# Kernel optimization log

Hardware: AMD Instinct MI355X
Metric: run time of the kernel (lower is better)

The kernel has to match this reference:

```python
import jax, jax.numpy as jnp
import numpy as np

B, N, C = 8, 4096, 640
H_HEADS = 5
HD = C // H_HEADS  # 128
KS = 5
FOCUS = 3.0
EPS = 1e-6


def setup_inputs() -> dict:
    key = jax.random.key(0)
    ks = jax.random.split(key, 12)
    s = 0.02
    return {
        "x1": jax.random.normal(ks[0], (B, N, C), jnp.float32),
        "x2": jax.random.normal(ks[1], (B, N, C), jnp.float32),
        "Wq": jax.random.normal(ks[2], (C, C), jnp.float32) * s,
        "Wkv": jax.random.normal(ks[3], (2 * C, C), jnp.float32) * s,
        "Wproj": jax.random.normal(ks[4], (C, C), jnp.float32) * s,
        "bproj": jax.random.normal(ks[5], (C,), jnp.float32) * s,
        "dwc_w": jax.random.normal(ks[6], (HD, 1, KS, KS), jnp.float32) * s,
        "dwc_b": jax.random.normal(ks[7], (HD,), jnp.float32) * s,
        "scale": jax.random.normal(ks[8], (1, 1, C), jnp.float32) * s,
        "pos_enc": jax.random.normal(ks[9], (1, N, C), jnp.float32) * s,
        "H": 64,
        "W": 64,
    }


def _split_heads(t):
    # [B, N, C] -> [(B*h), N, hd]
    b, n, c = t.shape
    return t.reshape(b, n, H_HEADS, HD).transpose(0, 2, 1, 3).reshape(b * H_HEADS, n, HD)


def reference(x1, x2, Wq, Wkv, Wproj, bproj, dwc_w, dwc_b, scale, pos_enc, H, W):
    b, n, c = x1.shape
    # note the module's naming swap: self.q projects x2 into v
    v = x2 @ Wq.T                               # [B,N,C]
    kv = (x1 @ Wkv.T).reshape(b, n, 2, c)       # sr_ratio == 1 path
    k = kv[:, :, 0, :] + pos_enc
    q = kv[:, :, 1, :]

    sc = jax.nn.softplus(scale)                 # [1,1,C]
    q = (jax.nn.relu(q) + EPS) / sc
    k = (jax.nn.relu(k) + EPS) / sc
    q_norm = jnp.linalg.norm(q, axis=-1, keepdims=True)
    k_norm = jnp.linalg.norm(k, axis=-1, keepdims=True)
    q = q ** FOCUS
    k = k ** FOCUS
    q = q / jnp.linalg.norm(q, axis=-1, keepdims=True) * q_norm
    k = k / jnp.linalg.norm(k, axis=-1, keepdims=True) * k_norm

    q, k, v = _split_heads(q), _split_heads(k), _split_heads(v)  # [(B*h), N, hd]
    i, j, cc, d = q.shape[-2], k.shape[-2], k.shape[-1], v.shape[-1]
    z = 1.0 / (jnp.einsum('bic,bc->bi', q, k.sum(axis=1)) + EPS)  # [(B*h), N]
    if i * j * (cc + d) > cc * d * (i + j):
        kv2 = jnp.einsum('bjc,bjd->bcd', k, v)                    # [(B*h), hd, hd]
        x = jnp.einsum('bic,bcd,bi->bid', q, kv2, z)
    else:
        qk = jnp.einsum('bic,bjc->bij', q, k)
        x = jnp.einsum('bij,bjd,bi->bid', qk, v, z)

    # depthwise conv feature map on v: 'b (w h) c -> b c w h'
    num = int(round(n ** 0.5))
    fm = v.reshape(v.shape[0], num, num, HD).transpose(0, 3, 1, 2)  # [(B*h), hd, num, num]
    fm = jax.lax.conv_general_dilated(
        fm, dwc_w, window_strides=(1, 1), padding=((KS // 2, KS // 2),) * 2,
        dimension_numbers=('NCHW', 'OIHW', 'NCHW'), feature_group_count=HD)
    fm = fm + dwc_b[None, :, None, None]
    fm = fm.transpose(0, 2, 3, 1).reshape(v.shape[0], n, HD)

    x = x + fm
    # '(b h) n c -> b n (h c)'
    x = x.reshape(b, H_HEADS, n, HD).transpose(0, 2, 1, 3).reshape(b, n, c)
    return x @ Wproj.T + bproj
```

## Files before the change

kernel.cpp:

```cpp
#include <hip/hip_runtime.h>
#include <math.h>

constexpr int CB  = 8;
constexpr int CN  = 4096;
constexpr int CC  = 640;
constexpr int CNH = 5;
constexpr int CHD = 128;
constexpr int CM  = CB * CN;
constexpr float CEPS = 1e-6f;
constexpr int NCH = 8;

typedef __attribute__((ext_vector_type(8))) short bf16x8;
typedef __attribute__((ext_vector_type(4))) float f32x4;

typedef __attribute__((address_space(1))) const unsigned int gas_u32;
typedef __attribute__((address_space(3))) unsigned int las_u32;

__device__ __forceinline__ void gload16(const void* g, void* l) {
    __builtin_amdgcn_global_load_lds((gas_u32*)g, (las_u32*)l, 16, 0, 0);
}

__device__ __forceinline__ short f2bf(float x) {
    unsigned u = __float_as_uint(x);
    unsigned r = (u + 0x7fffu + ((u >> 16) & 1u)) >> 16;
    return (short)r;
}
__device__ __forceinline__ float b2f(unsigned short u) {
    return __uint_as_float(((unsigned)u) << 16);
}

__device__ __forceinline__ void cvt8(const float* __restrict__ s, unsigned short* __restrict__ d) {
    float4 f0 = *(const float4*)s, f1 = *(const float4*)(s + 4);
    bf16x8 h;
    h[0]=f2bf(f0.x); h[1]=f2bf(f0.y); h[2]=f2bf(f0.z); h[3]=f2bf(f0.w);
    h[4]=f2bf(f1.x); h[5]=f2bf(f1.y); h[6]=f2bf(f1.z); h[7]=f2bf(f1.w);
    *(bf16x8*)d = h;
}

__global__ __launch_bounds__(256) void prep_weights(const float* __restrict__ scale,
                                                    const float* __restrict__ Wq,
                                                    const float* __restrict__ Wkv,
                                                    const float* __restrict__ Wproj,
                                                    float* __restrict__ sc,
                                                    unsigned short* __restrict__ Wqbf,
                                                    unsigned short* __restrict__ Wkvbf,
                                                    unsigned short* __restrict__ Wprojbf) {
    const int gid = blockIdx.x * 256 + threadIdx.x;
    if (gid < CC) sc[gid] = log1pf(expf(scale[gid]));
    const int NQ = CC * CC / 8;
    const int NKV = 2 * CC * CC / 8;
    const int total = NQ + NKV + NQ;
    const int stride = gridDim.x * 256;
    for (int c = gid; c < total; c += stride) {
        if (c < NQ)            cvt8(Wq    + (size_t)c * 8,            Wqbf    + (size_t)c * 8);
        else if (c < NQ + NKV) cvt8(Wkv   + (size_t)(c - NQ) * 8,     Wkvbf   + (size_t)(c - NQ) * 8);
        else                   cvt8(Wproj + (size_t)(c - NQ - NKV) * 8, Wprojbf + (size_t)(c - NQ - NKV) * 8);
    }
}

__global__ __launch_bounds__(256) void cvt_x12(const float* __restrict__ x1,
                                               const float* __restrict__ x2,
                                               unsigned short* __restrict__ x1bf,
                                               unsigned short* __restrict__ x2bf,
                                               int n8) {
    int i = blockIdx.x * 256 + threadIdx.x;
    const int stride = gridDim.x * 256;
    for (; i < 2 * n8; i += stride) {
        if (i < n8) cvt8(x1 + (size_t)i * 8,        x1bf + (size_t)i * 8);
        else        cvt8(x2 + (size_t)(i - n8) * 8, x2bf + (size_t)(i - n8) * 8);
    }
}

template<bool BIAS, bool OUTBF>
__device__ __forceinline__ void gemm_core(const unsigned short* __restrict__ Abf,
                                          const unsigned short* __restrict__ Bbf,
                                          void* __restrict__ Co,
                                          const float* __restrict__ bias,
                                          int Kr, int Nr, int wg, int npan, int mper) {
    __shared__ unsigned short lA[2][4096];
    __shared__ unsigned short lB[2][4096];
    const int t  = threadIdx.x;
    const int xcd  = wg & 7;
    const int j    = wg >> 3;
    const int m0 = (xcd * mper + j / npan) * 128;
    const int n0 = (j % npan) * 128;
    const int l  = t & 63, w = t >> 6, wr = w >> 1, wc = w & 1;

    const int cp0 = w * 64 + l;
    const int cp1 = cp0 + 256;
    const int s0 = cp0 ^ (((cp0 >> 2) & 7) ^ ((cp0 >> 4) & 1));
    const int s1 = cp1 ^ (((cp1 >> 2) & 7) ^ ((cp1 >> 4) & 1));
    const size_t gA0 = (size_t)(m0 + (s0 >> 2)) * Kr + (s0 & 3) * 8;
    const size_t gA1 = (size_t)(m0 + (s1 >> 2)) * Kr + (s1 & 3) * 8;
    const size_t gB0 = (size_t)(n0 + (s0 >> 2)) * Kr + (s0 & 3) * 8;
    const size_t gB1 = (size_t)(n0 + (s1 >> 2)) * Kr + (s1 & 3) * 8;
    const int dA0 = w * 512;
    const int dA1 = 2048 + w * 512;

    const int offA = ((wr * 64 + (l & 15)) * 64 + (l >> 4) * 16) ^ ((l & 7) << 4);
    const int offB = ((wc * 64 + (l & 15)) * 64 + (l >> 4) * 16) ^ ((l & 7) << 4);

    f32x4 acc[4][4];
    #pragma unroll
    for (int i = 0; i < 4; ++i)
        #pragma unroll
        for (int j2 = 0; j2 < 4; ++j2) acc[i][j2] = (f32x4){0.f, 0.f, 0.f, 0.f};

    gload16(Abf + gA0, &lA[0][dA0]);
    gload16(Abf + gA1, &lA[0][dA1]);
    gload16(Bbf + gB0, &lB[0][dA0]);
    gload16(Bbf + gB1, &lB[0][dA1]);
    __syncthreads();

    int cur = 0;
    for (int k0 = 0; k0 < Kr; k0 += 32) {
        if (k0 + 32 < Kr) {
            const int nb = cur ^ 1;
            gload16(Abf + gA0 + k0 + 32, &lA[nb][dA0]);
            gload16(Abf + gA1 + k0 + 32, &lA[nb][dA1]);
            gload16(Bbf + gB0 + k0 + 32, &lB[nb][dA0]);
            gload16(Bbf + gB1 + k0 + 32, &lB[nb][dA1]);
        }
        bf16x8 af[4], bfv[4];
        #pragma unroll
        for (int i = 0; i < 4; ++i) {
            af[i]  = *(const bf16x8*)((const char*)&lA[cur][0] + offA + i * 1024);
            bfv[i] = *(const bf16x8*)((const char*)&lB[cur][0] + offB + i * 1024);
        }
        #pragma unroll
        for (int i = 0; i < 4; ++i)
            #pragma unroll
            for (int j2 = 0; j2 < 4; ++j2)
                acc[i][j2] = __builtin_amdgcn_mfma_f32_16x16x32_bf16(af[i], bfv[j2], acc[i][j2], 0, 0, 0);
        __syncthreads();
        cur ^= 1;
    }

    #pragma unroll
    for (int j2 = 0; j2 < 4; ++j2) {
        const int n = n0 + wc * 64 + j2 * 16 + (l & 15);
        const float bv = BIAS ? bias[n] : 0.f;
        #pragma unroll
        for (int i = 0; i < 4; ++i) {
            const int m = m0 + wr * 64 + i * 16 + (l >> 4) * 4;
            #pragma unroll
            for (int r = 0; r < 4; ++r) {
                float val = acc[i][j2][r] + bv;
                if (OUTBF) ((unsigned short*)Co)[(size_t)(m + r) * Nr + n] = (unsigned short)f2bf(val);
                else       ((float*)Co)[(size_t)(m + r) * Nr + n] = val;
            }
        }
    }
}

__global__ __launch_bounds__(256) void gemm_vkq(const unsigned short* __restrict__ x2bf,
                                                const unsigned short* __restrict__ Wqbf,
                                                unsigned short* __restrict__ vbf,
                                                const unsigned short* __restrict__ x1bf,
                                                const unsigned short* __restrict__ Wkvbf,
                                                unsigned short* __restrict__ kqbf) {
    const int id = blockIdx.x;
    if (id < 1280) {
        gemm_core<false, true>(x2bf, Wqbf, (void*)vbf, nullptr, CC, CC, id, 5, 32);
    } else {
        gemm_core<false, true>(x1bf, Wkvbf, (void*)kqbf, nullptr, CC, 1280, id - 1280, 10, 32);
    }
}

__global__ __launch_bounds__(256) void gemm_proj(const unsigned short* __restrict__ xbf,
                                                 const unsigned short* __restrict__ Wprojbf,
                                                 float* __restrict__ out,
                                                 const float* __restrict__ bproj) {
    gemm_core<true, false>(xbf, Wprojbf, (void*)out, bproj, CC, CC,
                           blockIdx.y * gridDim.x + blockIdx.x, gridDim.x, gridDim.y >> 3);
}

__global__ __launch_bounds__(256) void rowtrans2(const unsigned short* __restrict__ kq,
                                                 const float* __restrict__ pos,
                                                 const float* __restrict__ sc,
                                                 unsigned short* __restrict__ qt,
                                                 unsigned short* __restrict__ kt) {
    const int w = threadIdx.x >> 6, l = threadIdx.x & 63;
    const int m = blockIdx.x * 4 + w;
    const int n = m & (CN - 1);
    const unsigned short* rowk = kq + (size_t)m * 1280;
    const unsigned short* rowq = rowk + 640;
    float qv[10], kv[10];
    float s2q = 0.f, s6q = 0.f, s2k = 0.f, s6k = 0.f;
    #pragma unroll
    for (int j = 0; j < 10; ++j) {
        const int c = l + 64 * j;
        const float scv = sc[c];
        float qq = (fmaxf(b2f(rowq[c]), 0.f) + CEPS) / scv;
        float kk = (fmaxf(b2f(rowk[c]) + pos[(size_t)n * CC + c], 0.f) + CEPS) / scv;
        qv[j] = qq; kv[j] = kk;
        const float q2 = qq * qq, k2 = kk * kk;
        s2q += q2; s6q += q2 * q2 * q2;
        s2k += k2; s6k += k2 * k2 * k2;
    }
    #pragma unroll
    for (int o = 32; o > 0; o >>= 1) {
        s2q += __shfl_xor(s2q, o);
        s6q += __shfl_xor(s6q, o);
        s2k += __shfl_xor(s2k, o);
        s6k += __shfl_xor(s6k, o);
    }
    const float qmul = sqrtf(s2q) / sqrtf(s6q);
    const float kmul = sqrtf(s2k) / sqrtf(s6k);
    #pragma unroll
    for (int j = 0; j < 10; ++j) {
        const int c = l + 64 * j;
        qt[(size_t)m * CC + c] = (unsigned short)f2bf(qv[j] * qv[j] * qv[j] * qmul);
        kt[(size_t)m * CC + c] = (unsigned short)f2bf(kv[j] * kv[j] * kv[j] * kmul);
    }
}

__global__ __launch_bounds__(256) void kv2_partial(const unsigned short* __restrict__ kt,
                                                   const unsigned short* __restrict__ vb,
                                                   float* __restrict__ kv2p,
                                                   float* __restrict__ ksmp) {
    const int nc = blockIdx.x, bh = blockIdx.y, q = blockIdx.z;
    const int qc = q & 1, qd = q >> 1;
    const int b = bh / CNH, h = bh % CNH;
    __shared__ float ks[32][68];
    __shared__ float vs[32][68];
    const int t = threadIdx.x;
    const int tx = t & 15, ty = t >> 4;
    float acc[4][4];
    #pragma unroll
    for (int i = 0; i < 4; ++i)
        #pragma unroll
        for (int j = 0; j < 4; ++j) acc[i][j] = 0.f;
    float ksacc = 0.f;
    const size_t mbase = (size_t)b * CN + (size_t)nc * 512;
    const int cofK = h * CHD + qc * 64;
    const int cofV = h * CHD + qd * 64;
    const int token = t >> 3, c8 = (t & 7) * 8;
    for (int tile = 0; tile < 16; ++tile) {
        const int nt0 = tile * 32;
        __syncthreads();
        {
            const size_t r = (mbase + nt0 + token) * CC;
            bf16x8 hk = *(const bf16x8*)(kt + r + cofK + c8);
            bf16x8 hv = *(const bf16x8*)(vb + r + cofV + c8);
            float4 k0, k1, v0, v1;
            k0.x=b2f(hk[0]); k0.y=b2f(hk[1]); k0.z=b2f(hk[2]); k0.w=b2f(hk[3]);
            k1.x=b2f(hk[4]); k1.y=b2f(hk[5]); k1.z=b2f(hk[6]); k1.w=b2f(hk[7]);
            v0.x=b2f(hv[0]); v0.y=b2f(hv[1]); v0.z=b2f(hv[2]); v0.w=b2f(hv[3]);
            v1.x=b2f(hv[4]); v1.y=b2f(hv[5]); v1.z=b2f(hv[6]); v1.w=b2f(hv[7]);
            *(float4*)&ks[token][c8]     = k0;
            *(float4*)&ks[token][c8 + 4] = k1;
            *(float4*)&vs[token][c8]     = v0;
            *(float4*)&vs[token][c8 + 4] = v1;
        }
        __syncthreads();
        #pragma unroll 4
        for (int nn = 0; nn < 32; ++nn) {
            float4 av = *(const float4*)&ks[nn][ty * 4];
            float4 bv = *(const float4*)&vs[nn][tx * 4];
            float a[4] = {av.x, av.y, av.z, av.w};
            float bb[4] = {bv.x, bv.y, bv.z, bv.w};
            #pragma unroll
            for (int i = 0; i < 4; ++i)
                #pragma unroll
                for (int j = 0; j < 4; ++j)
                    acc[i][j] = fmaf(a[i], bb[j], acc[i][j]);
        }
        if (qd == 0 && t < 64) {
            #pragma unroll
            for (int nn = 0; nn < 32; ++nn) ksacc += ks[nn][t];
        }
    }
    float* outp = kv2p + (((size_t)bh * NCH + nc) * 4 + q) * 4096;
    #pragma unroll
    for (int i = 0; i < 4; ++i) {
        float4 o;
        o.x = acc[i][0]; o.y = acc[i][1]; o.z = acc[i][2]; o.w = acc[i][3];
        *(float4*)&outp[(ty * 4 + i) * 64 + tx * 4] = o;
    }
    if (qd == 0 && t < 64)
        ksmp[(((size_t)bh * NCH + nc) * 2 + qc) * 64 + t] = ksacc;
}

__global__ __launch_bounds__(256) void kv2_reduce(const float* __restrict__ kv2p,
                                                  const float* __restrict__ ksmp,
                                                  unsigned short* __restrict__ kv2bf,
                                                  float* __restrict__ ksm) {
    const int bh = blockIdx.x, t = threadIdx.x;
    for (int o = t; o < 16384; o += 256) {
        const int d = o >> 7, c = o & 127;
        const int q = (d >> 6) * 2 + (c >> 6);
        float s = 0.f;
        #pragma unroll
        for (int nc = 0; nc < NCH; ++nc)
            s += kv2p[(((size_t)bh * NCH + nc) * 4 + q) * 4096 + (c & 63) * 64 + (d & 63)];
        kv2bf[(size_t)bh * 16384 + o] = (unsigned short)f2bf(s);
    }
    if (t < 128) {
        float s = 0.f;
        #pragma unroll
        for (int nc = 0; nc < NCH; ++nc)
            s += ksmp[(((size_t)bh * NCH + nc) * 2 + (t >> 6)) * 64 + (t & 63)];
        ksm[(size_t)bh * 128 + t] = s;
    }
}

__global__ __launch_bounds__(256) void attn_mfma(const unsigned short* __restrict__ qt,
                                                 const unsigned short* __restrict__ kv2bf,
                                                 const float* __restrict__ ksm,
                                                 unsigned short* __restrict__ attb) {
    const int nb = blockIdx.x, bh = blockIdx.y;
    const int b = bh / CNH, h = bh % CNH;
    __shared__ short lQ[16384];
    __shared__ short lKV[16384];
    __shared__ float zs[128];
    const int t = threadIdx.x;
    const int l = t & 63, w = t >> 6, wr = w >> 1, wc = w & 1;
    const size_t m0 = (size_t)b * CN + (size_t)nb * 128;

    const int srow0 = t >> 4;
    const int c16   = t & 15;
    float kreg[8];
    {
        const float* kp = ksm + (size_t)bh * 128 + c16 * 8;
        float4 k0 = *(const float4*)kp, k1 = *(const float4*)(kp + 4);
        kreg[0]=k0.x; kreg[1]=k0.y; kreg[2]=k0.z; kreg[3]=k0.w;
        kreg[4]=k1.x; kreg[5]=k1.y; kreg[6]=k1.z; kreg[7]=k1.w;
    }
    #pragma unroll
    for (int p = 0; p < 8; ++p) {
        const int row = srow0 + p * 16;
        const int st = (row * 256 + c16 * 16) ^ ((row & 7) << 4);
        bf16x8 hq = *(const bf16x8*)(qt + (m0 + row) * CC + h * CHD + c16 * 8);
        *(bf16x8*)((char*)lQ + st) = hq;
        float zp = 0.f;
        #pragma unroll
        for (int j = 0; j < 8; ++j) zp = fmaf(b2f((unsigned short)hq[j]), kreg[j], zp);
        zp += __shfl_xor(zp, 1);
        zp += __shfl_xor(zp, 2);
        zp += __shfl_xor(zp, 4);
        zp += __shfl_xor(zp, 8);
        if (c16 == 0) zs[row] = 1.f / (zp + CEPS);
        bf16x8 hk = *(const bf16x8*)(kv2bf + (size_t)bh * 16384 + row * 128 + c16 * 8);
        *(bf16x8*)((char*)lKV + st) = hk;
    }
    __syncthreads();

    const int baseA = (wr * 64 + (l & 15)) * 256 + ((l >> 4) << 4);
    const int baseB = (wc * 64 + (l & 15)) * 256 + ((l >> 4) << 4);
    const int xorv  = (l & 7) << 4;
    f32x4 acc[4][4];
    #pragma unroll
    for (int i = 0; i < 4; ++i)
        #pragma unroll
        for (int j = 0; j < 4; ++j) acc[i][j] = (f32x4){0.f, 0.f, 0.f, 0.f};

    #pragma unroll
    for (int kk = 0; kk < 4; ++kk) {
        bf16x8 af[4], bv[4];
        #pragma unroll
        for (int i = 0; i < 4; ++i) {
            af[i] = *(const bf16x8*)((const char*)lQ  + (((baseA + kk * 64) ^ xorv) + i * 4096));
            bv[i] = *(const bf16x8*)((const char*)lKV + (((baseB + kk * 64) ^ xorv) + i * 4096));
        }
        #pragma unroll
        for (int i = 0; i < 4; ++i)
            #pragma unroll
            for (int j = 0; j < 4; ++j)
                acc[i][j] = __builtin_amdgcn_mfma_f32_16x16x32_bf16(af[i], bv[j], acc[i][j], 0, 0, 0);
    }

    #pragma unroll
    for (int i = 0; i < 4; ++i) {
        const int mBase = wr * 64 + i * 16 + (l >> 4) * 4;
        float zv[4];
        #pragma unroll
        for (int r = 0; r < 4; ++r) zv[r] = zs[mBase + r];
        #pragma unroll
        for (int j = 0; j < 4; ++j) {
            const int n = wc * 64 + j * 16 + (l & 15);
            unsigned short* op = attb + (m0 + mBase) * CC + h * CHD + n;
            #pragma unroll
            for (int r = 0; r < 4; ++r)
                op[(size_t)r * CC] = (unsigned short)f2bf(acc[i][j][r] * zv[r]);
        }
    }
}

__global__ __launch_bounds__(256) void dwconv2(const unsigned short* __restrict__ vb,
                                               const unsigned short* __restrict__ attb,
                                               const float* __restrict__ w,
                                               const float* __restrict__ bias,
                                               unsigned short* __restrict__ xb) {
    const int yt = blockIdx.x;
    const int dq = blockIdx.y;
    const int bh = blockIdx.z;
    const int b = bh / CNH, h = bh % CNH;
    __shared__ unsigned short vt[12 * 68 * 32];
    const int t = threadIdx.x;
    const int y0 = yt * 8;
    const size_t rowbase = (size_t)b * CN;
    const int cbase = h * CHD + dq * 32;
    for (int c = t; c < 3264; c += 256) {
        int pos = c >> 2, d8 = (c & 3) * 8;
        int ly = pos / 68, lx = pos - ly * 68;
        int yy = y0 - 2 + ly, xx = lx - 2;
        bf16x8 val = (bf16x8){0,0,0,0,0,0,0,0};
        if (yy >= 0 && yy < 64 && xx >= 0 && xx < 64)
            val = *(const bf16x8*)(vb + (rowbase + yy * 64 + xx) * CC + cbase + d8);
        *(bf16x8*)(vt + pos * 32 + d8) = val;
    }
    __syncthreads();
    const int dp = t & 15;
    const int xg = t >> 4;
    const int d0 = dq * 32 + dp * 2;
    float wr0[25], wr1[25];
    #pragma unroll
    for (int i = 0; i < 25; ++i) {
        wr0[i] = w[d0 * 25 + i];
        wr1[i] = w[(d0 + 1) * 25 + i];
    }
    const float bv0 = bias[d0], bv1 = bias[d0 + 1];
    const int x0 = xg * 4;
    for (int oy = 0; oy < 8; ++oy) {
        float a0[4] = {bv0, bv0, bv0, bv0}, a1[4] = {bv1, bv1, bv1, bv1};
        #pragma unroll
        for (int dy = 0; dy < 5; ++dy) {
            const unsigned short* rp = vt + ((oy + dy) * 68 + x0) * 32 + dp * 2;
            float v0[8], v1[8];
            #pragma unroll
            for (int j = 0; j < 8; ++j) {
                unsigned pr = *(const unsigned*)(rp + j * 32);
                v0[j] = __uint_as_float(pr << 16);
                v1[j] = __uint_as_float(pr & 0xffff0000u);
            }
            #pragma unroll
            for (int dx = 0; dx < 5; ++dx) {
                const float w0 = wr0[dy * 5 + dx], w1 = wr1[dy * 5 + dx];
                #pragma unroll
                for (int xo = 0; xo < 4; ++xo) {
                    a0[xo] = fmaf(w0, v0[xo + dx], a0[xo]);
                    a1[xo] = fmaf(w1, v1[xo + dx], a1[xo]);
                }
            }
        }
        #pragma unroll
        for (int xo = 0; xo < 4; ++xo) {
            size_t g = (rowbase + (y0 + oy) * 64 + x0 + xo) * CC + cbase + dp * 2;
            unsigned ap = *(const unsigned*)(attb + g);
            float at0 = __uint_as_float(ap << 16);
            float at1 = __uint_as_float(ap & 0xffff0000u);
            unsigned short o0 = (unsigned short)f2bf(a0[xo] + at0);
            unsigned short o1 = (unsigned short)f2bf(a1[xo] + at1);
            *(unsigned*)(xb + g) = (unsigned)o0 | ((unsigned)o1 << 16);
        }
    }
}

extern "C" void kernel_launch(void* const* d_in, const int* in_sizes, int n_in,
                              void* d_out, int out_size, void* d_ws, size_t ws_size,
                              hipStream_t stream) {
    (void)in_sizes; (void)n_in; (void)out_size; (void)ws_size;
    const float* x1    = (const float*)d_in[0];
    const float* x2    = (const float*)d_in[1];
    const float* Wq    = (const float*)d_in[2];
    const float* Wkv   = (const float*)d_in[3];
    const float* Wproj = (const float*)d_in[4];
    const float* bproj = (const float*)d_in[5];
    const float* dwcw  = (const float*)d_in[6];
    const float* dwcb  = (const float*)d_in[7];
    const float* scale = (const float*)d_in[8];
    const float* pos   = (const float*)d_in[9];
    float* out = (float*)d_out;

    const size_t MC = (size_t)CM * CC;
    unsigned short* ws16 = (unsigned short*)d_ws;
    unsigned short* x1bf  = ws16;
    float*          kv2p  = (float*)ws16;
    unsigned short* attbf = ws16;
    unsigned short* x2bf = ws16 + MC;
    unsigned short* ktbf = x2bf;
    unsigned short* xbf  = x2bf;
    unsigned short* vbf  = ws16 + 2 * MC;
    unsigned short* qtbf = ws16 + 3 * MC;
    unsigned short* kv2bf = ws16 + 4 * MC;
    float* ksmp = (float*)(kv2bf + (size_t)40 * 16384);
    float* ksm  = ksmp + (size_t)40 * NCH * 128;
    float* scb  = ksm + (size_t)40 * 128;
    unsigned short* Wqbf    = (unsigned short*)(scb + 640);
    unsigned short* Wkvbf   = Wqbf + (size_t)CC * CC;
    unsigned short* Wprojbf = Wkvbf + (size_t)2 * CC * CC;
    unsigned short* kqbf = (unsigned short*)d_out;

    hipLaunchKernelGGL(prep_weights, dim3(256), dim3(256), 0, stream,
                       scale, Wq, Wkv, Wproj, scb, Wqbf, Wkvbf, Wprojbf);
    hipLaunchKernelGGL(cvt_x12, dim3(2048), dim3(256), 0, stream,
                       x1, x2, x1bf, x2bf, (int)(MC / 8));

    hipLaunchKernelGGL(gemm_vkq, dim3(3840), dim3(256), 0, stream,
                       x2bf, Wqbf, vbf, x1bf, Wkvbf, kqbf);
    hipLaunchKernelGGL(rowtrans2, dim3(CM/4), dim3(256), 0, stream, kqbf, pos, scb, qtbf, ktbf);
    hipLaunchKernelGGL(kv2_partial, dim3(NCH, 40, 4), dim3(256), 0, stream, ktbf, vbf, kv2p, ksmp);
    hipLaunchKernelGGL(kv2_reduce, dim3(40), dim3(256), 0, stream, kv2p, ksmp, kv2bf, ksm);
    hipLaunchKernelGGL(attn_mfma, dim3(CN/128, 40), dim3(256), 0, stream, qtbf, kv2bf, ksm, attbf);
    hipLaunchKernelGGL(dwconv2, dim3(8, 4, 40), dim3(256), 0, stream, vbf, attbf, dwcw, dwcb, xbf);
    hipLaunchKernelGGL(gemm_proj, dim3(CC/128, CM/128), dim3(256), 0, stream,
                       xbf, Wprojbf, out, bproj);
}
```

Measured before the change: 479.7 us.

## Fuse q/k feature-map transform into consumers, store only per-row norm factors

```diff
diff --git a/kernel.cpp b/kernel.cpp
--- a/kernel.cpp
+++ b/kernel.cpp
@@ -175,17 +175,16 @@
                            blockIdx.y * gridDim.x + blockIdx.x, gridDim.x, gridDim.y >> 3);
 }
 
-__global__ __launch_bounds__(256) void rowtrans2(const unsigned short* __restrict__ kq,
-                                                 const float* __restrict__ pos,
-                                                 const float* __restrict__ sc,
-                                                 unsigned short* __restrict__ qt,
-                                                 unsigned short* __restrict__ kt) {
+__global__ __launch_bounds__(256) void rowfact(const unsigned short* __restrict__ kq,
+                                               const float* __restrict__ pos,
+                                               const float* __restrict__ sc,
+                                               float* __restrict__ qf,
+                                               float* __restrict__ kf) {
     const int w = threadIdx.x >> 6, l = threadIdx.x & 63;
     const int m = blockIdx.x * 4 + w;
     const int n = m & (CN - 1);
     const unsigned short* rowk = kq + (size_t)m * 1280;
     const unsigned short* rowq = rowk + 640;
-    float qv[10], kv[10];
     float s2q = 0.f, s6q = 0.f, s2k = 0.f, s6k = 0.f;
     #pragma unroll
     for (int j = 0; j < 10; ++j) {
@@ -193,7 +192,6 @@
         const float scv = sc[c];
         float qq = (fmaxf(b2f(rowq[c]), 0.f) + CEPS) / scv;
         float kk = (fmaxf(b2f(rowk[c]) + pos[(size_t)n * CC + c], 0.f) + CEPS) / scv;
-        qv[j] = qq; kv[j] = kk;
         const float q2 = qq * qq, k2 = kk * kk;
         s2q += q2; s6q += q2 * q2 * q2;
         s2k += k2; s6k += k2 * k2 * k2;
@@ -205,18 +203,17 @@
         s2k += __shfl_xor(s2k, o);
         s6k += __shfl_xor(s6k, o);
     }
-    const float qmul = sqrtf(s2q) / sqrtf(s6q);
-    const float kmul = sqrtf(s2k) / sqrtf(s6k);
-    #pragma unroll
-    for (int j = 0; j < 10; ++j) {
-        const int c = l + 64 * j;
-        qt[(size_t)m * CC + c] = (unsigned short)f2bf(qv[j] * qv[j] * qv[j] * qmul);
-        kt[(size_t)m * CC + c] = (unsigned short)f2bf(kv[j] * kv[j] * kv[j] * kmul);
-    }
-}
-
-__global__ __launch_bounds__(256) void kv2_partial(const unsigned short* __restrict__ kt,
+    if (l == 0) {
+        qf[m] = sqrtf(s2q) / sqrtf(s6q);
+        kf[m] = sqrtf(s2k) / sqrtf(s6k);
+    }
+}
+
+__global__ __launch_bounds__(256) void kv2_partial(const unsigned short* __restrict__ kqb,
                                                    const unsigned short* __restrict__ vb,
+                                                   const float* __restrict__ pos,
+                                                   const float* __restrict__ sc,
+                                                   const float* __restrict__ kf,
                                                    float* __restrict__ kv2p,
                                                    float* __restrict__ ksmp) {
     const int nc = blockIdx.x, bh = blockIdx.y, q = blockIdx.z;
@@ -236,18 +233,34 @@
     const int cofK = h * CHD + qc * 64;
     const int cofV = h * CHD + qd * 64;
     const int token = t >> 3, c8 = (t & 7) * 8;
+    float scv[8];
+    #pragma unroll
+    for (int e = 0; e < 8; ++e) scv[e] = sc[cofK + c8 + e];
     for (int tile = 0; tile < 16; ++tile) {
         const int nt0 = tile * 32;
         __syncthreads();
         {
-            const size_t r = (mbase + nt0 + token) * CC;
-            bf16x8 hk = *(const bf16x8*)(kt + r + cofK + c8);
-            bf16x8 hv = *(const bf16x8*)(vb + r + cofV + c8);
+            const size_t m = mbase + nt0 + token;
+            const int n = (int)(m & (CN - 1));
+            bf16x8 hk = *(const bf16x8*)(kqb + m * 1280 + cofK + c8);
+            bf16x8 hv = *(const bf16x8*)(vb + m * CC + cofV + c8);
+            const float kmul = kf[m];
+            float4 p0 = *(const float4*)(pos + (size_t)n * CC + cofK + c8);
+            float4 p1 = *(const float4*)(pos + (size_t)n * CC + cofK + c8 + 4);
+            float pe[8] = {p0.x, p0.y, p0.z, p0.w, p1.x, p1.y, p1.z, p1.w};
+            float kkv[8];
+            #pragma unroll
+            for (int e = 0; e < 8; ++e) {
+                float kk = (fmaxf(b2f((unsigned short)hk[e]) + pe[e], 0.f) + CEPS) / scv[e];
+                kkv[e] = kk * kk * kk * kmul;
+            }
             float4 k0, k1, v0, v1;
-            k0.x=b2f(hk[0]); k0.y=b2f(hk[1]); k0.z=b2f(hk[2]); k0.w=b2f(hk[3]);
-            k1.x=b2f(hk[4]); k1.y=b2f(hk[5]); k1.z=b2f(hk[6]); k1.w=b2f(hk[7]);
-            v0.x=b2f(hv[0]); v0.y=b2f(hv[1]); v0.z=b2f(hv[2]); v0.w=b2f(hv[3]);
-            v1.x=b2f(hv[4]); v1.y=b2f(hv[5]); v1.z=b2f(hv[6]); v1.w=b2f(hv[7]);
+            k0.x=kkv[0]; k0.y=kkv[1]; k0.z=kkv[2]; k0.w=kkv[3];
+            k1.x=kkv[4]; k1.y=kkv[5]; k1.z=kkv[6]; k1.w=kkv[7];
+            v0.x=b2f((unsigned short)hv[0]); v0.y=b2f((unsigned short)hv[1]);
+            v0.z=b2f((unsigned short)hv[2]); v0.w=b2f((unsigned short)hv[3]);
+            v1.x=b2f((unsigned short)hv[4]); v1.y=b2f((unsigned short)hv[5]);
+            v1.z=b2f((unsigned short)hv[6]); v1.w=b2f((unsigned short)hv[7]);
             *(float4*)&ks[token][c8]     = k0;
             *(float4*)&ks[token][c8 + 4] = k1;
             *(float4*)&vs[token][c8]     = v0;
@@ -305,7 +318,9 @@
     }
 }
 
-__global__ __launch_bounds__(256) void attn_mfma(const unsigned short* __restrict__ qt,
+__global__ __launch_bounds__(256) void attn_mfma(const unsigned short* __restrict__ kqb,
+                                                 const float* __restrict__ sc,
+                                                 const float* __restrict__ qf,
                                                  const unsigned short* __restrict__ kv2bf,
                                                  const float* __restrict__ ksm,
                                                  unsigned short* __restrict__ attb) {
@@ -320,22 +335,33 @@
 
     const int srow0 = t >> 4;
     const int c16   = t & 15;
-    float kreg[8];
+    float kreg[8], scv[8];
     {
         const float* kp = ksm + (size_t)bh * 128 + c16 * 8;
         float4 k0 = *(const float4*)kp, k1 = *(const float4*)(kp + 4);
         kreg[0]=k0.x; kreg[1]=k0.y; kreg[2]=k0.z; kreg[3]=k0.w;
         kreg[4]=k1.x; kreg[5]=k1.y; kreg[6]=k1.z; kreg[7]=k1.w;
+        #pragma unroll
+        for (int e = 0; e < 8; ++e) scv[e] = sc[h * CHD + c16 * 8 + e];
     }
     #pragma unroll
     for (int p = 0; p < 8; ++p) {
         const int row = srow0 + p * 16;
         const int st = (row * 256 + c16 * 16) ^ ((row & 7) << 4);
-        bf16x8 hq = *(const bf16x8*)(qt + (m0 + row) * CC + h * CHD + c16 * 8);
+        bf16x8 hraw = *(const bf16x8*)(kqb + (m0 + row) * 1280 + 640 + h * CHD + c16 * 8);
+        const float qmul = qf[m0 + row];
+        float qv[8];
+        bf16x8 hq;
+        #pragma unroll
+        for (int e = 0; e < 8; ++e) {
+            float qq = (fmaxf(b2f((unsigned short)hraw[e]), 0.f) + CEPS) / scv[e];
+            qv[e] = qq * qq * qq * qmul;
+            hq[e] = f2bf(qv[e]);
+        }
         *(bf16x8*)((char*)lQ + st) = hq;
         float zp = 0.f;
         #pragma unroll
-        for (int j = 0; j < 8; ++j) zp = fmaf(b2f((unsigned short)hq[j]), kreg[j], zp);
+        for (int j = 0; j < 8; ++j) zp = fmaf(qv[j], kreg[j], zp);
         zp += __shfl_xor(zp, 1);
         zp += __shfl_xor(zp, 2);
         zp += __shfl_xor(zp, 4);
@@ -479,10 +505,8 @@
     float*          kv2p  = (float*)ws16;
     unsigned short* attbf = ws16;
     unsigned short* x2bf = ws16 + MC;
-    unsigned short* ktbf = x2bf;
     unsigned short* xbf  = x2bf;
     unsigned short* vbf  = ws16 + 2 * MC;
-    unsigned short* qtbf = ws16 + 3 * MC;
     unsigned short* kv2bf = ws16 + 4 * MC;
     float* ksmp = (float*)(kv2bf + (size_t)40 * 16384);
     float* ksm  = ksmp + (size_t)40 * NCH * 128;
@@ -490,6 +514,8 @@
     unsigned short* Wqbf    = (unsigned short*)(scb + 640);
     unsigned short* Wkvbf   = Wqbf + (size_t)CC * CC;
     unsigned short* Wprojbf = Wkvbf + (size_t)2 * CC * CC;
+    float* qf = (float*)(Wprojbf + (size_t)CC * CC);
+    float* kf = qf + CM;
     unsigned short* kqbf = (unsigned short*)d_out;
 
     hipLaunchKernelGGL(prep_weights, dim3(256), dim3(256), 0, stream,
@@ -499,10 +525,12 @@
 
     hipLaunchKernelGGL(gemm_vkq, dim3(3840), dim3(256), 0, stream,
                        x2bf, Wqbf, vbf, x1bf, Wkvbf, kqbf);
-    hipLaunchKernelGGL(rowtrans2, dim3(CM/4), dim3(256), 0, stream, kqbf, pos, scb, qtbf, ktbf);
-    hipLaunchKernelGGL(kv2_partial, dim3(NCH, 40, 4), dim3(256), 0, stream, ktbf, vbf, kv2p, ksmp);
+    hipLaunchKernelGGL(rowfact, dim3(CM/4), dim3(256), 0, stream, kqbf, pos, scb, qf, kf);
+    hipLaunchKernelGGL(kv2_partial, dim3(NCH, 40, 4), dim3(256), 0, stream,
+                       kqbf, vbf, pos, scb, kf, kv2p, ksmp);
     hipLaunchKernelGGL(kv2_reduce, dim3(40), dim3(256), 0, stream, kv2p, ksmp, kv2bf, ksm);
-    hipLaunchKernelGGL(attn_mfma, dim3(CN/128, 40), dim3(256), 0, stream, qtbf, kv2bf, ksm, attbf);
+    hipLaunchKernelGGL(attn_mfma, dim3(CN/128, 40), dim3(256), 0, stream,
+                       kqbf, scb, qf, kv2bf, ksm, attbf);
     hipLaunchKernelGGL(dwconv2, dim3(8, 4, 40), dim3(256), 0, stream, vbf, attbf, dwcw, dwcb, xbf);
     hipLaunchKernelGGL(gemm_proj, dim3(CC/128, CM/128), dim3(256), 0, stream,
                        xbf, Wprojbf, out, bproj);
```

After: 494.8 us. +3.2%, slower.
